# Optimization experiments

Measured on AMD Instinct MI355X. Metric: run time of the kernel, lower is better.

The kernel has to match this reference:

```python
import jax, jax.numpy as jnp
import numpy as np

N_NODES = 100000
NEG_SLOPE = 0.01  # F.leaky_relu default


def _hetero_graphconv(x, src, dst, W, b, n_nodes):
    """HeteroGraphConv(aggregate='sum') of DGL GraphConv(norm='both') per edge type.

    x: [N, d_in]; src/dst: [R, E] int; W: [R, d_in, d_out]; b: [R, d_out].
    """
    n_rel = W.shape[0]
    ones = None
    out = jnp.zeros((n_nodes, W.shape[2]), dtype=x.dtype)
    for r in range(n_rel):  # small fixed number of relations
        s, d = src[r], dst[r]
        e_ones = jnp.ones(s.shape, dtype=x.dtype)
        deg_out = jnp.clip(jax.ops.segment_sum(e_ones, s, num_segments=n_nodes), 1.0)
        deg_in = jnp.clip(jax.ops.segment_sum(e_ones, d, num_segments=n_nodes), 1.0)
        # norm='both': scale src by out_deg^-1/2, aggregate, scale dst by in_deg^-1/2.
        # Apply weight before gather (aggregation is linear) to shrink edge traffic.
        h = (x * (deg_out ** -0.5)[:, None]) @ W[r]          # [N, d_out]
        agg = jax.ops.segment_sum(h[s], d, num_segments=n_nodes)  # gather-scatter over edges
        out = out + agg * (deg_in ** -0.5)[:, None] + b[r]
    return out


def setup_inputs() -> dict:
    key = jax.random.key(0)
    ks = jax.random.split(key, 8)
    d_in, d_h, d_out, n_cls, n_rel, n_edges = 256, 128, 128, 16, 3, 600000
    x = jax.random.normal(ks[0], (N_NODES, d_in), dtype=jnp.float32)
    src = jax.random.randint(ks[1], (n_rel, n_edges), 0, N_NODES, dtype=jnp.int32)
    dst = jax.random.randint(ks[2], (n_rel, n_edges), 0, N_NODES, dtype=jnp.int32)
    W0 = jax.random.normal(ks[3], (n_rel, d_in, d_h), dtype=jnp.float32) * (d_in ** -0.5)
    b0 = jnp.zeros((n_rel, d_h), dtype=jnp.float32)
    W1 = jax.random.normal(ks[4], (n_rel, d_h, d_out), dtype=jnp.float32) * (d_h ** -0.5)
    b1 = jnp.zeros((n_rel, d_out), dtype=jnp.float32)
    fc_W = jax.random.normal(ks[5], (d_out, n_cls), dtype=jnp.float32) * (d_out ** -0.5)
    fc_b = jnp.zeros((n_cls,), dtype=jnp.float32)
    return {"x": x, "src": src, "dst": dst, "W0": W0, "b0": b0,
            "W1": W1, "b1": b1, "fc_W": fc_W, "fc_b": fc_b}


def reference(x, src, dst, W0, b0, W1, b1, fc_W, fc_b):
    n = x.shape[0]
    h = _hetero_graphconv(x, src, dst, W0, b0, n)
    h = jax.nn.leaky_relu(h, negative_slope=NEG_SLOPE)  # dropout rate 0 (eval)
    h = _hetero_graphconv(h, src, dst, W1, b1, n)       # last layer: no activation
    logits = h @ fc_W + fc_b
    return (h, logits)
```

## Files before the change

### kernel.cpp

```cpp
#include <hip/hip_runtime.h>
#include <hip/hip_bf16.h>
#include <stdint.h>


typedef __attribute__((ext_vector_type(8))) short bf16x8;
typedef __attribute__((ext_vector_type(4))) float f32x4;
typedef unsigned short u16;

#define CUR_PAD 16
#define BF_K 8
#define CAP 32

__global__ __launch_bounds__(256)
void bucket_hist(const int* __restrict__ src, const int* __restrict__ dst,
                 int* __restrict__ cnt_out, int* __restrict__ cursor,
                 int* __restrict__ bkt, int E, int N) {
    int r = blockIdx.y;
    int e0 = blockIdx.x * (256 * BF_K) + threadIdx.x;
    int s[BF_K], d[BF_K], pos[BF_K];
#pragma unroll
    for (int j = 0; j < BF_K; j++) {
        int e = e0 + j * 256;
        bool v = e < E;
        s[j] = v ? src[(size_t)r * E + e] : -1;
        d[j] = v ? dst[(size_t)r * E + e] : 0;
    }
#pragma unroll
    for (int j = 0; j < BF_K; j++)
        if (s[j] >= 0)
            atomicAdd(cnt_out + ((size_t)s[j] * 3 + r) * CUR_PAD, 1);
#pragma unroll
    for (int j = 0; j < BF_K; j++)
        pos[j] = (s[j] >= 0)
               ? atomicAdd(cursor + ((size_t)d[j] * 3 + r) * CUR_PAD, 1) : 0;
#pragma unroll
    for (int j = 0; j < BF_K; j++)
        if (s[j] >= 0 && pos[j] < CAP)
            bkt[((size_t)d[j] * 3 + r) * CAP + pos[j]] = r * N + s[j];
}

__global__ __launch_bounds__(256)
void reduce_scales_kernel(const int* __restrict__ cnt_out, const int* __restrict__ cursor,
                          float* __restrict__ s_out, float* __restrict__ s_in, int N) {
    int n = blockIdx.x * blockDim.x + threadIdx.x;
    if (n >= N) return;
#pragma unroll
    for (int r = 0; r < 3; r++) {
        int co = cnt_out[((size_t)n * 3 + r) * CUR_PAD];
        s_out[(size_t)r * N + n] = rsqrtf(fmaxf((float)co, 1.0f));
        int ci = cursor[((size_t)n * 3 + r) * CUR_PAD];
        s_in[(size_t)r * N + n] = rsqrtf(fmaxf((float)ci, 1.0f));
    }
}

__global__ __launch_bounds__(256)
void prep_w_kernel(const float* __restrict__ W0, const float* __restrict__ W1,
                   u16* __restrict__ w0hi, u16* __restrict__ w0lo,
                   u16* __restrict__ w1hi, u16* __restrict__ w1lo) {
    int idx = blockIdx.x * blockDim.x + threadIdx.x;
    const int n0 = 3 * 256 * 128;
    const int n1 = 3 * 128 * 128;
    if (idx >= n0 + n1) return;
    float f;
    u16 *phi, *plo;
    int oidx;
    if (idx < n0) {
        int r = idx / 32768, rem = idx % 32768;
        int n = rem / 256, k = rem % 256;
        f = W0[(size_t)r * 32768 + (size_t)k * 128 + n];
        phi = w0hi; plo = w0lo; oidx = idx;
    } else {
        int i2 = idx - n0;
        int r = i2 / 16384, rem = i2 % 16384;
        int n = rem / 128, k = rem % 128;
        f = W1[(size_t)r * 16384 + (size_t)k * 128 + n];
        phi = w1hi; plo = w1lo; oidx = i2;
    }
    uint32_t u = __float_as_uint(f);
    phi[oidx] = (u16)(u >> 16);
    float lo = f - __uint_as_float(u & 0xFFFF0000u);
    uint32_t ul = __float_as_uint(lo);
    plo[oidx] = (u16)((ul + 0x7FFFu + ((ul >> 16) & 1u)) >> 16);
}

__global__ __launch_bounds__(256)
void gemm_split_bf16(const float* __restrict__ A, const float* __restrict__ s_out,
                     const u16* __restrict__ Whi_all, const u16* __restrict__ Wlo_all,
                     u16* __restrict__ Cout_all, int M, int K, int Nn) {
    const int r = blockIdx.y;
    const float* scale = s_out + (size_t)r * Nn;
    const u16* Whi = Whi_all + (size_t)r * K * 128;
    const u16* Wlo = Wlo_all + (size_t)r * K * 128;
    u16* Cout = Cout_all + (size_t)r * Nn * 128;

    __shared__ u16 As_hi[128][40];
    __shared__ u16 As_lo[128][40];
    __shared__ u16 Bs_hi[128][40];
    __shared__ u16 Bs_lo[128][40];

    const int tid  = threadIdx.x;
    const int m0   = blockIdx.x * 128;
    const int lane = tid & 63;
    const int wave = tid >> 6;
    const int wm   = (wave & 1) * 64;
    const int wn   = (wave >> 1) * 64;
    const int lm   = lane & 15;
    const int kq   = (lane >> 4) * 8;

    f32x4 acc[4][4];
#pragma unroll
    for (int i = 0; i < 4; i++)
#pragma unroll
        for (int j = 0; j < 4; j++) acc[i][j] = (f32x4){0.f, 0.f, 0.f, 0.f};

    const int srow = tid >> 1;
    const int skb  = (tid & 1) * 16;

    const bool valid = (m0 + srow) < M;
    const float sval = valid ? scale[m0 + srow] : 0.f;
    const float* arow = A + (size_t)(m0 + srow) * K;
    const u16* whrow = Whi + (size_t)srow * K;
    const u16* wlrow = Wlo + (size_t)srow * K;

    for (int k0 = 0; k0 < K; k0 += 32) {
        float fa[16];
        if (valid) {
            *(float4*)&fa[0]  = *(const float4*)(arow + k0 + skb);
            *(float4*)&fa[4]  = *(const float4*)(arow + k0 + skb + 4);
            *(float4*)&fa[8]  = *(const float4*)(arow + k0 + skb + 8);
            *(float4*)&fa[12] = *(const float4*)(arow + k0 + skb + 12);
        } else {
#pragma unroll
            for (int i = 0; i < 16; i++) fa[i] = 0.f;
        }
        uint32_t ah[8], al[8];
#pragma unroll
        for (int p = 0; p < 8; p++) {
            float f0 = fa[2 * p] * sval, f1 = fa[2 * p + 1] * sval;
            uint32_t u0 = __float_as_uint(f0), u1 = __float_as_uint(f1);
            ah[p] = (u0 >> 16) | (u1 & 0xFFFF0000u);
            float l0 = f0 - __uint_as_float(u0 & 0xFFFF0000u);
            float l1 = f1 - __uint_as_float(u1 & 0xFFFF0000u);
            al[p] = (__float_as_uint(l0) >> 16) | (__float_as_uint(l1) & 0xFFFF0000u);
        }
        *(uint4*)&As_hi[srow][skb]     = *(uint4*)&ah[0];
        *(uint4*)&As_hi[srow][skb + 8] = *(uint4*)&ah[4];
        *(uint4*)&As_lo[srow][skb]     = *(uint4*)&al[0];
        *(uint4*)&As_lo[srow][skb + 8] = *(uint4*)&al[4];

        *(uint4*)&Bs_hi[srow][skb]     = *(const uint4*)(whrow + k0 + skb);
        *(uint4*)&Bs_hi[srow][skb + 8] = *(const uint4*)(whrow + k0 + skb + 8);
        *(uint4*)&Bs_lo[srow][skb]     = *(const uint4*)(wlrow + k0 + skb);
        *(uint4*)&Bs_lo[srow][skb + 8] = *(const uint4*)(wlrow + k0 + skb + 8);

        __syncthreads();

        bf16x8 a_hi[4], a_lo[4], b_hi[4], b_lo[4];
#pragma unroll
        for (int i = 0; i < 4; i++) {
            a_hi[i] = *(const bf16x8*)&As_hi[wm + i * 16 + lm][kq];
            a_lo[i] = *(const bf16x8*)&As_lo[wm + i * 16 + lm][kq];
            b_hi[i] = *(const bf16x8*)&Bs_hi[wn + i * 16 + lm][kq];
            b_lo[i] = *(const bf16x8*)&Bs_lo[wn + i * 16 + lm][kq];
        }
#pragma unroll
        for (int i = 0; i < 4; i++)
#pragma unroll
            for (int j = 0; j < 4; j++) {
                acc[i][j] = __builtin_amdgcn_mfma_f32_16x16x32_bf16(a_hi[i], b_hi[j], acc[i][j], 0, 0, 0);
                acc[i][j] = __builtin_amdgcn_mfma_f32_16x16x32_bf16(a_lo[i], b_hi[j], acc[i][j], 0, 0, 0);
                acc[i][j] = __builtin_amdgcn_mfma_f32_16x16x32_bf16(a_hi[i], b_lo[j], acc[i][j], 0, 0, 0);
            }
        __syncthreads();
    }

    const int rq = (lane >> 4) * 4;
#pragma unroll
    for (int i = 0; i < 4; i++) {
        int mbase = m0 + wm + i * 16 + rq;
#pragma unroll
        for (int j = 0; j < 4; j++) {
            int col = wn + j * 16 + lm;
#pragma unroll
            for (int rg = 0; rg < 4; rg++) {
                int m = mbase + rg;
                if (m < M) {
                    uint32_t u = __float_as_uint(acc[i][j][rg]);
                    Cout[(size_t)m * 128 + col] =
                        (u16)((u + 0x7FFFu + ((u >> 16) & 1u)) >> 16);
                }
            }
        }
    }
}

#define BF16_LO(u) __uint_as_float((u) << 16)
#define BF16_HI(u) __uint_as_float((u) & 0xFFFF0000u)

__device__ __forceinline__ void gather_all(const uint32_t* __restrict__ hb32,
                                           const int* __restrict__ cursor,
                                           const int* __restrict__ bkt,
                                           const float* __restrict__ s_in,
                                           int node, int lane, int N,
                                           float& ox, float& oy) {
    const uint32_t* hrow = hb32 + lane;
    int d0 = __builtin_amdgcn_readfirstlane(cursor[(size_t)node * (3 * CUR_PAD)]);
    int d1 = __builtin_amdgcn_readfirstlane(cursor[(size_t)node * (3 * CUR_PAD) + CUR_PAD]);
    int d2 = __builtin_amdgcn_readfirstlane(cursor[(size_t)node * (3 * CUR_PAD) + 2 * CUR_PAD]);
    d0 = d0 > CAP ? CAP : d0;
    d1 = d1 > CAP ? CAP : d1;
    d2 = d2 > CAP ? CAP : d2;
    const int t01 = d0 + d1;
    const int tot = t01 + d2;
    const int* bp = bkt + (size_t)node * (3 * CAP);
    const float w0 = s_in[node];
    const float w1 = s_in[(size_t)N + node];
    const float w2 = s_in[(size_t)2 * N + node];
    float ax = 0.f, ay = 0.f, bx = 0.f, by = 0.f;
    float cx = 0.f, cy = 0.f, dx = 0.f, dy = 0.f;
    for (int j = 0; j < tot; j += 8) {
        uint32_t u[8];
        float w[8];
#pragma unroll
        for (int p = 0; p < 8; p++) {
            int jj = j + p;
            int r2 = (jj >= d0 ? 1 : 0) + (jj >= t01 ? 1 : 0);
            int off = r2 == 0 ? 0 : (r2 == 1 ? d0 - CAP : t01 - 2 * CAP);
            int bval = bp[jj - off];
            bool act = jj < tot;
            int idx = act ? bval : 0;
            float ws = r2 == 0 ? w0 : (r2 == 1 ? w1 : w2);
            w[p] = act ? ws : 0.f;
            u[p] = hrow[(size_t)idx * 64];
        }
#pragma unroll
        for (int p = 0; p < 8; p += 4) {
            ax = fmaf(BF16_LO(u[p]),     w[p],     ax);
            ay = fmaf(BF16_HI(u[p]),     w[p],     ay);
            bx = fmaf(BF16_LO(u[p + 1]), w[p + 1], bx);
            by = fmaf(BF16_HI(u[p + 1]), w[p + 1], by);
            cx = fmaf(BF16_LO(u[p + 2]), w[p + 2], cx);
            cy = fmaf(BF16_HI(u[p + 2]), w[p + 2], cy);
            dx = fmaf(BF16_LO(u[p + 3]), w[p + 3], dx);
            dy = fmaf(BF16_HI(u[p + 3]), w[p + 3], dy);
        }
    }
    ox = (ax + bx) + (cx + dx);
    oy = (ay + by) + (cy + dy);
}

__global__ __launch_bounds__(256)
void gather_l0(const u16* __restrict__ hb, const int* __restrict__ cursor,
               const int* __restrict__ bkt, const float* __restrict__ s_in,
               const float* __restrict__ b, float* __restrict__ out, int N) {
    int node = blockIdx.x * 4 + (threadIdx.x >> 6);
    if (node >= N) return;
    int lane = threadIdx.x & 63;
    float tx, ty;
    gather_all((const uint32_t*)hb, cursor, bkt, s_in, node, lane, N, tx, ty);
    int c0 = lane * 2;
    tx += b[c0] + b[128 + c0] + b[256 + c0];
    ty += b[c0 + 1] + b[128 + c0 + 1] + b[256 + c0 + 1];
    tx = fmaxf(tx, 0.f) + 0.01f * fminf(tx, 0.f);
    ty = fmaxf(ty, 0.f) + 0.01f * fminf(ty, 0.f);
    *(float2*)(out + (size_t)node * 128 + c0) = make_float2(tx, ty);
}

__global__ __launch_bounds__(256)
void gather_l1(const u16* __restrict__ hb, const int* __restrict__ cursor,
               const int* __restrict__ bkt, const float* __restrict__ s_in,
               const float* __restrict__ b, const float* __restrict__ fcW,
               const float* __restrict__ fcb, float* __restrict__ out_h,
               float* __restrict__ out_logits, int N) {
    int node = blockIdx.x * 4 + (threadIdx.x >> 6);
    if (node >= N) return;
    int lane = threadIdx.x & 63;
    float tx, ty;
    gather_all((const uint32_t*)hb, cursor, bkt, s_in, node, lane, N, tx, ty);
    int c0 = lane * 2;
    tx += b[c0] + b[128 + c0] + b[256 + c0];
    ty += b[c0 + 1] + b[128 + c0 + 1] + b[256 + c0 + 1];
    *(float2*)(out_h + (size_t)node * 128 + c0) = make_float2(tx, ty);

    const float* fc0 = fcW + (size_t)c0 * 16;
    float p[16];
#pragma unroll
    for (int j = 0; j < 16; j++) p[j] = tx * fc0[j] + ty * fc0[16 + j];
#pragma unroll
    for (int off = 1; off < 64; off <<= 1) {
#pragma unroll
        for (int j = 0; j < 16; j++) p[j] += __shfl_xor(p[j], off);
    }
    if (lane == 0) {
        float* lp = out_logits + (size_t)node * 16;
        *(float4*)(lp + 0)  = make_float4(p[0] + fcb[0],  p[1] + fcb[1],  p[2] + fcb[2],  p[3] + fcb[3]);
        *(float4*)(lp + 4)  = make_float4(p[4] + fcb[4],  p[5] + fcb[5],  p[6] + fcb[6],  p[7] + fcb[7]);
        *(float4*)(lp + 8)  = make_float4(p[8] + fcb[8],  p[9] + fcb[9],  p[10] + fcb[10], p[11] + fcb[11]);
        *(float4*)(lp + 12) = make_float4(p[12] + fcb[12], p[13] + fcb[13], p[14] + fcb[14], p[15] + fcb[15]);
    }
}

extern "C" void kernel_launch(void* const* d_in, const int* in_sizes, int n_in,
                              void* d_out, int out_size, void* d_ws, size_t ws_size,
                              hipStream_t stream) {
    const float* x   = (const float*)d_in[0];
    const int*   src = (const int*)d_in[1];
    const int*   dst = (const int*)d_in[2];
    const float* W0  = (const float*)d_in[3];
    const float* b0  = (const float*)d_in[4];
    const float* W1  = (const float*)d_in[5];
    const float* b1  = (const float*)d_in[6];
    const float* fcW = (const float*)d_in[7];
    const float* fcb = (const float*)d_in[8];

    const int N = in_sizes[0] / 256;
    const int E = in_sizes[1] / 3;

    float* out_h      = (float*)d_out;
    float* out_logits = out_h + (size_t)N * 128;

    char* p = (char*)d_ws;
    auto alloc = [&](size_t bytes) -> char* {
        char* q = p;
        p += (bytes + 255) & ~(size_t)255;
        return q;
    };
    float* s_out     = (float*)alloc(3 * (size_t)N * 4);
    float* s_in      = (float*)alloc(3 * (size_t)N * 4);
    int*   cnt_out   = (int*)alloc(3 * (size_t)N * CUR_PAD * 4);
    int*   cursor    = (int*)alloc(3 * (size_t)N * CUR_PAD * 4);
    int*   bkt       = (int*)alloc(3 * (size_t)N * CAP * 4 + 1024);
    u16*   w0hi      = (u16*)alloc(3 * 256 * 128 * 2);
    u16*   w0lo      = (u16*)alloc(3 * 256 * 128 * 2);
    u16*   w1hi      = (u16*)alloc(3 * 128 * 128 * 2);
    u16*   w1lo      = (u16*)alloc(3 * 128 * 128 * 2);
    u16*   hb        = (u16*)alloc(3 * (size_t)N * 128 * 2);
    float* acc0      = (float*)alloc((size_t)N * 128 * 4);

    hipMemsetAsync(cnt_out, 0, 2 * 3 * (size_t)N * CUR_PAD * sizeof(int), stream);

    bucket_hist<<<dim3((E + 256 * BF_K - 1) / (256 * BF_K), 3), 256, 0, stream>>>(
        src, dst, cnt_out, cursor, bkt, E, N);
    reduce_scales_kernel<<<(N + 255) / 256, 256, 0, stream>>>(
        cnt_out, cursor, s_out, s_in, N);

    prep_w_kernel<<<(3 * 256 * 128 + 3 * 128 * 128 + 255) / 256, 256, 0, stream>>>(
        W0, W1, w0hi, w0lo, w1hi, w1lo);

    int gemm_blocks   = (N + 127) / 128;
    int gather_blocks = (N + 3) / 4;

    gemm_split_bf16<<<dim3(gemm_blocks, 3), 256, 0, stream>>>(
        x, s_out, w0hi, w0lo, hb, N, 256, N);
    gather_l0<<<gather_blocks, 256, 0, stream>>>(hb, cursor, bkt, s_in, b0, acc0, N);

    gemm_split_bf16<<<dim3(gemm_blocks, 3), 256, 0, stream>>>(
        acc0, s_out, w1hi, w1lo, hb, N, 128, N);
    gather_l1<<<gather_blocks, 256, 0, stream>>>(hb, cursor, bkt, s_in, b1, fcW, fcb,
                                                 out_h, out_logits, N);
}
```

Before: 729.3 us.

## Fuse edge bucketing into layer-0 GEMM launch and defer source-degree scaling to gather

The layer-0 GEMM no longer depends on out-degree scaling, since s_out is now applied per edge inside the layer-0 gather. That lets the edge histogram and bucketing run as extra block roles in the same launch as the GEMM, so the atomic-heavy bucketing can overlap with the MFMA work instead of running in its own launch beforehand. The cost is an extra s_out load for every gathered edge in layer 0. Block scheduling order also decides how well the two roles actually overlap.

```diff
diff --git a/kernel.cpp b/kernel.cpp
--- a/kernel.cpp
+++ b/kernel.cpp
@@ -12,31 +12,146 @@
 #define CAP 32
 
 __global__ __launch_bounds__(256)
-void bucket_hist(const int* __restrict__ src, const int* __restrict__ dst,
-                 int* __restrict__ cnt_out, int* __restrict__ cursor,
-                 int* __restrict__ bkt, int E, int N) {
-    int r = blockIdx.y;
-    int e0 = blockIdx.x * (256 * BF_K) + threadIdx.x;
-    int s[BF_K], d[BF_K], pos[BF_K];
-#pragma unroll
-    for (int j = 0; j < BF_K; j++) {
-        int e = e0 + j * 256;
-        bool v = e < E;
-        s[j] = v ? src[(size_t)r * E + e] : -1;
-        d[j] = v ? dst[(size_t)r * E + e] : 0;
-    }
-#pragma unroll
-    for (int j = 0; j < BF_K; j++)
-        if (s[j] >= 0)
-            atomicAdd(cnt_out + ((size_t)s[j] * 3 + r) * CUR_PAD, 1);
-#pragma unroll
-    for (int j = 0; j < BF_K; j++)
-        pos[j] = (s[j] >= 0)
-               ? atomicAdd(cursor + ((size_t)d[j] * 3 + r) * CUR_PAD, 1) : 0;
-#pragma unroll
-    for (int j = 0; j < BF_K; j++)
-        if (s[j] >= 0 && pos[j] < CAP)
-            bkt[((size_t)d[j] * 3 + r) * CAP + pos[j]] = r * N + s[j];
+void gemm0_bucket(const float* __restrict__ A,
+                  const u16* __restrict__ Whi_all, const u16* __restrict__ Wlo_all,
+                  u16* __restrict__ Cout_all, int M, int K, int Nn,
+                  const int* __restrict__ src, const int* __restrict__ dst,
+                  int* __restrict__ cnt_out, int* __restrict__ cursor,
+                  int* __restrict__ bkt, int E, int N) {
+    __shared__ u16 As_hi[128][40];
+    __shared__ u16 As_lo[128][40];
+    __shared__ u16 Bs_hi[128][40];
+    __shared__ u16 Bs_lo[128][40];
+
+    const int role = blockIdx.x;
+
+    if (role >= 3) {
+        const int r = role - 3;
+        const int nbk = (E + 256 * BF_K - 1) / (256 * BF_K);
+        const int b = blockIdx.y;
+        if (b >= nbk) return;
+        int e0 = b * (256 * BF_K) + threadIdx.x;
+        int s[BF_K], d[BF_K], pos[BF_K];
+#pragma unroll
+        for (int j = 0; j < BF_K; j++) {
+            int e = e0 + j * 256;
+            bool v = e < E;
+            s[j] = v ? src[(size_t)r * E + e] : -1;
+            d[j] = v ? dst[(size_t)r * E + e] : 0;
+        }
+#pragma unroll
+        for (int j = 0; j < BF_K; j++)
+            if (s[j] >= 0)
+                atomicAdd(cnt_out + ((size_t)s[j] * 3 + r) * CUR_PAD, 1);
+#pragma unroll
+        for (int j = 0; j < BF_K; j++)
+            pos[j] = (s[j] >= 0)
+                   ? atomicAdd(cursor + ((size_t)d[j] * 3 + r) * CUR_PAD, 1) : 0;
+#pragma unroll
+        for (int j = 0; j < BF_K; j++)
+            if (s[j] >= 0 && pos[j] < CAP)
+                bkt[((size_t)d[j] * 3 + r) * CAP + pos[j]] = r * N + s[j];
+        return;
+    }
+
+    const int r = role;
+    const u16* Whi = Whi_all + (size_t)r * K * 128;
+    const u16* Wlo = Wlo_all + (size_t)r * K * 128;
+    u16* Cout = Cout_all + (size_t)r * Nn * 128;
+
+    const int tid  = threadIdx.x;
+    const int m0   = blockIdx.y * 128;
+    const int lane = tid & 63;
+    const int wave = tid >> 6;
+    const int wm   = (wave & 1) * 64;
+    const int wn   = (wave >> 1) * 64;
+    const int lm   = lane & 15;
+    const int kq   = (lane >> 4) * 8;
+
+    f32x4 acc[4][4];
+#pragma unroll
+    for (int i = 0; i < 4; i++)
+#pragma unroll
+        for (int j = 0; j < 4; j++) acc[i][j] = (f32x4){0.f, 0.f, 0.f, 0.f};
+
+    const int srow = tid >> 1;
+    const int skb  = (tid & 1) * 16;
+
+    const bool valid = (m0 + srow) < M;
+    const float* arow = A + (size_t)(m0 + srow) * K;
+    const u16* whrow = Whi + (size_t)srow * K;
+    const u16* wlrow = Wlo + (size_t)srow * K;
+
+    for (int k0 = 0; k0 < K; k0 += 32) {
+        float fa[16];
+        if (valid) {
+            *(float4*)&fa[0]  = *(const float4*)(arow + k0 + skb);
+            *(float4*)&fa[4]  = *(const float4*)(arow + k0 + skb + 4);
+            *(float4*)&fa[8]  = *(const float4*)(arow + k0 + skb + 8);
+            *(float4*)&fa[12] = *(const float4*)(arow + k0 + skb + 12);
+        } else {
+#pragma unroll
+            for (int i = 0; i < 16; i++) fa[i] = 0.f;
+        }
+        uint32_t ah[8], al[8];
+#pragma unroll
+        for (int p = 0; p < 8; p++) {
+            float f0 = fa[2 * p], f1 = fa[2 * p + 1];
+            uint32_t u0 = __float_as_uint(f0), u1 = __float_as_uint(f1);
+            ah[p] = (u0 >> 16) | (u1 & 0xFFFF0000u);
+            float l0 = f0 - __uint_as_float(u0 & 0xFFFF0000u);
+            float l1 = f1 - __uint_as_float(u1 & 0xFFFF0000u);
+            al[p] = (__float_as_uint(l0) >> 16) | (__float_as_uint(l1) & 0xFFFF0000u);
+        }
+        *(uint4*)&As_hi[srow][skb]     = *(uint4*)&ah[0];
+        *(uint4*)&As_hi[srow][skb + 8] = *(uint4*)&ah[4];
+        *(uint4*)&As_lo[srow][skb]     = *(uint4*)&al[0];
+        *(uint4*)&As_lo[srow][skb + 8] = *(uint4*)&al[4];
+
+        *(uint4*)&Bs_hi[srow][skb]     = *(const uint4*)(whrow + k0 + skb);
+        *(uint4*)&Bs_hi[srow][skb + 8] = *(const uint4*)(whrow + k0 + skb + 8);
+        *(uint4*)&Bs_lo[srow][skb]     = *(const uint4*)(wlrow + k0 + skb);
+        *(uint4*)&Bs_lo[srow][skb + 8] = *(const uint4*)(wlrow + k0 + skb + 8);
+
+        __syncthreads();
+
+        bf16x8 a_hi[4], a_lo[4], b_hi[4], b_lo[4];
+#pragma unroll
+        for (int i = 0; i < 4; i++) {
+            a_hi[i] = *(const bf16x8*)&As_hi[wm + i * 16 + lm][kq];
+            a_lo[i] = *(const bf16x8*)&As_lo[wm + i * 16 + lm][kq];
+            b_hi[i] = *(const bf16x8*)&Bs_hi[wn + i * 16 + lm][kq];
+            b_lo[i] = *(const bf16x8*)&Bs_lo[wn + i * 16 + lm][kq];
+        }
+#pragma unroll
+        for (int i = 0; i < 4; i++)
+#pragma unroll
+            for (int j = 0; j < 4; j++) {
+                acc[i][j] = __builtin_amdgcn_mfma_f32_16x16x32_bf16(a_hi[i], b_hi[j], acc[i][j], 0, 0, 0);
+                acc[i][j] = __builtin_amdgcn_mfma_f32_16x16x32_bf16(a_lo[i], b_hi[j], acc[i][j], 0, 0, 0);
+                acc[i][j] = __builtin_amdgcn_mfma_f32_16x16x32_bf16(a_hi[i], b_lo[j], acc[i][j], 0, 0, 0);
+            }
+        __syncthreads();
+    }
+
+    const int rq = (lane >> 4) * 4;
+#pragma unroll
+    for (int i = 0; i < 4; i++) {
+        int mbase = m0 + wm + i * 16 + rq;
+#pragma unroll
+        for (int j = 0; j < 4; j++) {
+            int col = wn + j * 16 + lm;
+#pragma unroll
+            for (int rg = 0; rg < 4; rg++) {
+                int m = mbase + rg;
+                if (m < M) {
+                    uint32_t u = __float_as_uint(acc[i][j][rg]);
+                    Cout[(size_t)m * 128 + col] =
+                        (u16)((u + 0x7FFFu + ((u >> 16) & 1u)) >> 16);
+                }
+            }
+        }
+    }
 }
 
 __global__ __launch_bounds__(256)
@@ -197,10 +312,12 @@
 #define BF16_LO(u) __uint_as_float((u) << 16)
 #define BF16_HI(u) __uint_as_float((u) & 0xFFFF0000u)
 
+template<bool SOUT>
 __device__ __forceinline__ void gather_all(const uint32_t* __restrict__ hb32,
                                            const int* __restrict__ cursor,
                                            const int* __restrict__ bkt,
                                            const float* __restrict__ s_in,
+                                           const float* __restrict__ s_out,
                                            int node, int lane, int N,
                                            float& ox, float& oy) {
     const uint32_t* hrow = hb32 + lane;
@@ -230,6 +347,7 @@
             bool act = jj < tot;
             int idx = act ? bval : 0;
             float ws = r2 == 0 ? w0 : (r2 == 1 ? w1 : w2);
+            if (SOUT) ws *= s_out[idx];
             w[p] = act ? ws : 0.f;
             u[p] = hrow[(size_t)idx * 64];
         }
@@ -252,12 +370,13 @@
 __global__ __launch_bounds__(256)
 void gather_l0(const u16* __restrict__ hb, const int* __restrict__ cursor,
                const int* __restrict__ bkt, const float* __restrict__ s_in,
+               const float* __restrict__ s_out,
                const float* __restrict__ b, float* __restrict__ out, int N) {
     int node = blockIdx.x * 4 + (threadIdx.x >> 6);
     if (node >= N) return;
     int lane = threadIdx.x & 63;
     float tx, ty;
-    gather_all((const uint32_t*)hb, cursor, bkt, s_in, node, lane, N, tx, ty);
+    gather_all<true>((const uint32_t*)hb, cursor, bkt, s_in, s_out, node, lane, N, tx, ty);
     int c0 = lane * 2;
     tx += b[c0] + b[128 + c0] + b[256 + c0];
     ty += b[c0 + 1] + b[128 + c0 + 1] + b[256 + c0 + 1];
@@ -276,7 +395,7 @@
     if (node >= N) return;
     int lane = threadIdx.x & 63;
     float tx, ty;
-    gather_all((const uint32_t*)hb, cursor, bkt, s_in, node, lane, N, tx, ty);
+    gather_all<false>((const uint32_t*)hb, cursor, bkt, s_in, nullptr, node, lane, N, tx, ty);
     int c0 = lane * 2;
     tx += b[c0] + b[128 + c0] + b[256 + c0];
     ty += b[c0 + 1] + b[128 + c0 + 1] + b[256 + c0 + 1];
@@ -339,20 +458,19 @@
 
     hipMemsetAsync(cnt_out, 0, 2 * 3 * (size_t)N * CUR_PAD * sizeof(int), stream);
 
-    bucket_hist<<<dim3((E + 256 * BF_K - 1) / (256 * BF_K), 3), 256, 0, stream>>>(
-        src, dst, cnt_out, cursor, bkt, E, N);
+    prep_w_kernel<<<(3 * 256 * 128 + 3 * 128 * 128 + 255) / 256, 256, 0, stream>>>(
+        W0, W1, w0hi, w0lo, w1hi, w1lo);
+
+    int gemm_blocks   = (N + 127) / 128;
+    int gather_blocks = (N + 3) / 4;
+
+    gemm0_bucket<<<dim3(6, gemm_blocks), 256, 0, stream>>>(
+        x, w0hi, w0lo, hb, N, 256, N, src, dst, cnt_out, cursor, bkt, E, N);
+
     reduce_scales_kernel<<<(N + 255) / 256, 256, 0, stream>>>(
         cnt_out, cursor, s_out, s_in, N);
 
-    prep_w_kernel<<<(3 * 256 * 128 + 3 * 128 * 128 + 255) / 256, 256, 0, stream>>>(
-        W0, W1, w0hi, w0lo, w1hi, w1lo);
-
-    int gemm_blocks   = (N + 127) / 128;
-    int gather_blocks = (N + 3) / 4;
-
-    gemm_split_bf16<<<dim3(gemm_blocks, 3), 256, 0, stream>>>(
-        x, s_out, w0hi, w0lo, hb, N, 256, N);
-    gather_l0<<<gather_blocks, 256, 0, stream>>>(hb, cursor, bkt, s_in, b0, acc0, N);
+    gather_l0<<<gather_blocks, 256, 0, stream>>>(hb, cursor, bkt, s_in, s_out, b0, acc0, N);
 
     gemm_split_bf16<<<dim3(gemm_blocks, 3), 256, 0, stream>>>(
         acc0, s_out, w1hi, w1lo, hb, N, 128, N);
```

After: 695.2 us. -4.7%, faster.
